# Kernel optimization log

Hardware: AMD Instinct MI355X
Metric: run time of the kernel (lower is better)

The kernel has to match this reference:

```python
import jax, jax.numpy as jnp
import numpy as np

B, N, C = 4, 1024, 1024
H = 16
HD = C // H
FF = 4 * C
EPS = 1e-6


def layernorm(x, g, b):
    mu = jnp.mean(x, axis=-1, keepdims=True)
    var = jnp.mean((x - mu) ** 2, axis=-1, keepdims=True)
    return (x - mu) * jax.lax.rsqrt(var + EPS) * g + b


def setup_inputs() -> dict:
    key = jax.random.key(0)
    ks = jax.random.split(key, 16)
    s = lambda fan_in: 1.0 / np.sqrt(fan_in)
    inp = {
        "x": jax.random.normal(ks[0], (B, N, C), dtype=jnp.float32),
        "qkv_w": jax.random.normal(ks[1], (3 * C, C), dtype=jnp.float32) * s(C),
        "qkv_b": jnp.zeros((3 * C,), jnp.float32),
        "attn_proj_w": jax.random.normal(ks[2], (C, C), dtype=jnp.float32) * s(C),
        "attn_proj_b": jnp.zeros((C,), jnp.float32),
        "blk_proj_w": jax.random.normal(ks[3], (C, C), dtype=jnp.float32) * s(C),
        "blk_proj_b": jnp.zeros((C,), jnp.float32),
        "ln1_g": jnp.ones((C,), jnp.float32),
        "ln1_b": jnp.zeros((C,), jnp.float32),
        "ln2_g": jnp.ones((C,), jnp.float32),
        "ln2_b": jnp.zeros((C,), jnp.float32),
        "fc1_w": jax.random.normal(ks[4], (FF, C), dtype=jnp.float32) * s(C),
        "fc1_b": jnp.zeros((FF,), jnp.float32),
        "fc2_w": jax.random.normal(ks[5], (C, FF), dtype=jnp.float32) * s(FF),
        "fc2_b": jnp.zeros((C,), jnp.float32),
        "mask": jnp.ones((B, N), jnp.int32),  # unused by the original forward
    }
    return inp


def reference(x, qkv_w, qkv_b, attn_proj_w, attn_proj_b, blk_proj_w, blk_proj_b,
              ln1_g, ln1_b, ln2_g, ln2_b, fc1_w, fc1_b, fc2_w, fc2_b, mask):
    shortcut = x
    xn = layernorm(x, ln1_g, ln1_b)

    # QKV projection: [B,N,3C] -> [3,B,H,N,HD]
    qkv = xn @ qkv_w.T + qkv_b
    qkv = qkv.reshape(B, N, 3, H, HD).transpose(2, 0, 3, 1, 4)
    q, k, v = qkv[0], qkv[1], qkv[2]
    scale = HD ** -0.5
    attn = jnp.einsum('bhqd,bhkd->bhqk', q * scale, k)
    attn = jax.nn.softmax(attn, axis=-1)
    o = jnp.einsum('bhqk,bhkd->bhqd', attn, v)
    o = o.transpose(0, 2, 1, 3).reshape(B, N, C)
    o = o @ attn_proj_w.T + attn_proj_b  # attention-internal proj

    x = shortcut + (o @ blk_proj_w.T + blk_proj_b)  # Block's extra proj + residual

    h = layernorm(x, ln2_g, ln2_b)
    h = jax.nn.gelu(h @ fc1_w.T + fc1_b, approximate=False)
    h = h @ fc2_w.T + fc2_b
    return x + h
```

## Files before the change

kernel.cpp:

```cpp
#include <hip/hip_runtime.h>

typedef unsigned short u16;
typedef __attribute__((ext_vector_type(8))) short short8;
typedef __attribute__((ext_vector_type(4))) float f32x4;

#define DEVI __device__ __forceinline__

static constexpr int Nn = 1024;
static constexpr int Cc = 1024;

DEVI u16 f2bf(float f) {
  union { float f; unsigned u; } v; v.f = f;
  unsigned r = v.u + 0x7fffu + ((v.u >> 16) & 1u);
  return (u16)(r >> 16);
}

DEVI void async_ld16(const void* g, void* lds) {
  __builtin_amdgcn_global_load_lds(
      (__attribute__((address_space(1))) void*)g,
      (__attribute__((address_space(3))) void*)lds, 16, 0, 0);
}

__global__ __launch_bounds__(256) void cvt_all(
    const float* __restrict__ s0, const float* __restrict__ s1,
    const float* __restrict__ s2, const float* __restrict__ s3,
    const float* __restrict__ s4, u16* __restrict__ out) {
  const size_t i = ((size_t)blockIdx.x * 256 + threadIdx.x) * 4;
  const float* src; size_t lo;
  if (i < 3145728)      { src = s0; lo = 0; }
  else if (i < 4194304) { src = s1; lo = 3145728; }
  else if (i < 5242880) { src = s2; lo = 4194304; }
  else if (i < 9437184) { src = s3; lo = 5242880; }
  else                  { src = s4; lo = 9437184; }
  const float4 v = *(const float4*)&src[i - lo];
  ushort4 o;
  o.x = f2bf(v.x); o.y = f2bf(v.y); o.z = f2bf(v.z); o.w = f2bf(v.w);
  *(ushort4*)&out[i] = o;
}

__global__ __launch_bounds__(256) void transpose_wT(const float* __restrict__ in,
                                                    u16* __restrict__ out) {
  __shared__ u16 tile[64][72];
  const int bx = blockIdx.x & 15, by = blockIdx.x >> 4;
  const int tr = threadIdx.x >> 2;
  const int tc4 = (threadIdx.x & 3) * 16;
#pragma unroll
  for (int j = 0; j < 4; ++j) {
    const float4 v = *(const float4*)&in[(size_t)(by * 64 + tr) * 1024 +
                                         bx * 64 + tc4 + j * 4];
    tile[tc4 + j * 4 + 0][tr] = f2bf(v.x);
    tile[tc4 + j * 4 + 1][tr] = f2bf(v.y);
    tile[tc4 + j * 4 + 2][tr] = f2bf(v.z);
    tile[tc4 + j * 4 + 3][tr] = f2bf(v.w);
  }
  __syncthreads();
#pragma unroll
  for (int j = 0; j < 4; ++j) {
    ushort4 o;
    o.x = tile[tr][tc4 + j * 4 + 0];
    o.y = tile[tr][tc4 + j * 4 + 1];
    o.z = tile[tr][tc4 + j * 4 + 2];
    o.w = tile[tr][tc4 + j * 4 + 3];
    *(ushort4*)&out[(size_t)(bx * 64 + tr) * 1024 + by * 64 + tc4 + j * 4] = o;
  }
}

__global__ __launch_bounds__(256) void cbias_k(const float* __restrict__ apb,
                                               const float* __restrict__ bpw,
                                               const float* __restrict__ bpb,
                                               float* __restrict__ cb) {
  const int j = blockIdx.x * 4 + (threadIdx.x >> 6);
  const int lane = threadIdx.x & 63;
  float s = 0.f;
  for (int k = lane; k < 1024; k += 64) s += apb[k] * bpw[(size_t)j * 1024 + k];
#pragma unroll
  for (int m = 1; m < 64; m <<= 1) s += __shfl_xor(s, m);
  if (lane == 0) cb[j] = s + bpb[j];
}

__global__ __launch_bounds__(256) void gemm64(const u16* __restrict__ A,
                                              const u16* __restrict__ W,
                                              u16* __restrict__ out, int K) {
  __shared__ __align__(16) u16 As[64 * 64];
  __shared__ __align__(16) u16 Bs[64 * 64];
  const int tid = threadIdx.x;
  const int wave = tid >> 6, lane = tid & 63;
  const int g = lane >> 4, lr = lane & 15;
  const int brow = (blockIdx.x >> 4) << 6, bcol = (blockIdx.x & 15) << 6;
  const int srow = lane >> 3;
  const int scg = (lane & 7) ^ srow;
  const int swz = (lr & 7) << 4;

  f32x4 acc[4];
#pragma unroll
  for (int j = 0; j < 4; ++j) acc[j] = (f32x4){0.f, 0.f, 0.f, 0.f};

  for (int k0 = 0; k0 < K; k0 += 64) {
#pragma unroll
    for (int u = 0; u < 2; ++u) {
      async_ld16(A + (size_t)(brow + u * 32 + wave * 8 + srow) * K + k0 + scg * 8,
                 (char*)As + u * 4096 + wave * 1024);
      async_ld16(W + (size_t)(bcol + u * 32 + wave * 8 + srow) * K + k0 + scg * 8,
                 (char*)Bs + u * 4096 + wave * 1024);
    }
    __syncthreads();
    short8 af[2], bf[4][2];
#pragma unroll
    for (int kk = 0; kk < 2; ++kk)
      af[kk] = *(const short8*)((char*)As + (wave * 16 + lr) * 128 +
                                ((kk * 64 + g * 16) ^ swz));
#pragma unroll
    for (int nf = 0; nf < 4; ++nf)
#pragma unroll
      for (int kk = 0; kk < 2; ++kk)
        bf[nf][kk] = *(const short8*)((char*)Bs + (nf * 16 + lr) * 128 +
                                      ((kk * 64 + g * 16) ^ swz));
#pragma unroll
    for (int nf = 0; nf < 4; ++nf)
#pragma unroll
      for (int kk = 0; kk < 2; ++kk)
        acc[nf] = __builtin_amdgcn_mfma_f32_16x16x32_bf16(af[kk], bf[nf][kk],
                                                          acc[nf], 0, 0, 0);
    __syncthreads();
  }
#pragma unroll
  for (int nf = 0; nf < 4; ++nf)
#pragma unroll
    for (int reg = 0; reg < 4; ++reg)
      out[(size_t)(brow + wave * 16 + g * 4 + reg) * 1024 +
          bcol + nf * 16 + lr] = f2bf(acc[nf][reg]);
}

__global__ __launch_bounds__(256) void vtrans(const u16* __restrict__ qkv,
                                              u16* __restrict__ vt) {
  __shared__ u16 tile[64][72];
  const int bh = blockIdx.x >> 4, tb = blockIdx.x & 15;
  const int b = bh >> 4, h = bh & 15;
  const int t0 = tb * 64;
  const int tid = threadIdx.x;
  const int rr = tid >> 3, c8 = (tid & 7) * 8;
#pragma unroll
  for (int r = 0; r < 2; ++r) {
    const int t = r * 32 + rr;
    const short8 v = *(const short8*)(qkv + (size_t)(b * Nn + t0 + t) * 3072 +
                                      2048 + h * 64 + c8);
#pragma unroll
    for (int j = 0; j < 8; ++j) tile[t][c8 + j] = (u16)v[j];
  }
  __syncthreads();
#pragma unroll
  for (int r = 0; r < 2; ++r) {
    const int d = r * 32 + rr;
    short8 o;
#pragma unroll
    for (int j = 0; j < 8; ++j) o[j] = (short)tile[c8 + j][d];
    *(short8*)(vt + (size_t)(bh * 64 + d) * 1024 + t0 + c8) = o;
  }
}

__global__ __launch_bounds__(256) void ln_bf16(const float* __restrict__ x,
                                               const float* __restrict__ gg,
                                               const float* __restrict__ bb,
                                               u16* __restrict__ out) {
  const int row = blockIdx.x;
  const float4 v = ((const float4*)(x + (size_t)row * 1024))[threadIdx.x];
  float s  = v.x + v.y + v.z + v.w;
  float s2 = v.x * v.x + v.y * v.y + v.z * v.z + v.w * v.w;
#pragma unroll
  for (int m = 1; m < 64; m <<= 1) { s += __shfl_xor(s, m); s2 += __shfl_xor(s2, m); }
  __shared__ float ps[4], ps2[4];
  const int wave = threadIdx.x >> 6;
  if ((threadIdx.x & 63) == 0) { ps[wave] = s; ps2[wave] = s2; }
  __syncthreads();
  s = ps[0] + ps[1] + ps[2] + ps[3];
  s2 = ps2[0] + ps2[1] + ps2[2] + ps2[3];
  const float mu = s * (1.0f / 1024.0f);
  const float var = s2 * (1.0f / 1024.0f) - mu * mu;
  const float rs = rsqrtf(var + 1e-6f);
  const float4 gv = ((const float4*)gg)[threadIdx.x];
  const float4 bv = ((const float4*)bb)[threadIdx.x];
  ushort4 o;
  o.x = f2bf((v.x - mu) * rs * gv.x + bv.x);
  o.y = f2bf((v.y - mu) * rs * gv.y + bv.y);
  o.z = f2bf((v.z - mu) * rs * gv.z + bv.z);
  o.w = f2bf((v.w - mu) * rs * gv.w + bv.w);
  ((ushort4*)(out + (size_t)row * 1024))[threadIdx.x] = o;
}

template <bool GELU_, bool OUTBF>
__global__ __launch_bounds__(512, 4) void gemmS(
    const u16* __restrict__ A, const u16* __restrict__ W,
    const float* __restrict__ bias, void* __restrict__ out,
    int M, int N, int K) {
  __shared__ __align__(16) u16 As[256 * 64];
  __shared__ __align__(16) u16 Bs[128 * 64];
  const int tid = threadIdx.x;
  const int wave = tid >> 6, lane = tid & 63;
  const int g = lane >> 4, lr = lane & 15;
  const int wm = wave >> 1, wn = wave & 1;
  const int ntile = N >> 7;
  const int nwg = gridDim.x;
  int bid = blockIdx.x;
  bid = (bid & 7) * (nwg >> 3) + (bid >> 3);
  const int brow = (bid / ntile) << 8, bcol = (bid % ntile) << 7;

  const int sru = wave * 8 + (lane >> 3);
  const int scg = (lane & 7) ^ (lane >> 3);
  const int swz = (lr & 7) << 4;

  f32x4 acc[4][4];
#pragma unroll
  for (int i = 0; i < 4; ++i)
#pragma unroll
    for (int j = 0; j < 4; ++j) acc[i][j] = (f32x4){0.f, 0.f, 0.f, 0.f};

  for (int k0 = 0; k0 < K; k0 += 64) {
#pragma unroll
    for (int u = 0; u < 2; ++u)
      async_ld16(W + (size_t)(bcol + u * 64 + sru) * K + k0 + scg * 8,
                 (char*)Bs + u * 8192 + wave * 1024);
#pragma unroll
    for (int u = 0; u < 4; ++u)
      async_ld16(A + (size_t)(brow + u * 64 + sru) * K + k0 + scg * 8,
                 (char*)As + u * 8192 + wave * 1024);
    asm volatile("s_waitcnt vmcnt(0)" ::: "memory");
    __builtin_amdgcn_s_barrier();

    short8 bf[4][2];
#pragma unroll
    for (int nf = 0; nf < 4; ++nf) {
      const int row = wn * 64 + nf * 16 + lr;
#pragma unroll
      for (int kk = 0; kk < 2; ++kk)
        bf[nf][kk] = *(const short8*)((const char*)Bs + row * 128 +
                                      ((kk * 64 + g * 16) ^ swz));
    }
    __builtin_amdgcn_s_setprio(1);
#pragma unroll
    for (int mf = 0; mf < 4; ++mf) {
      short8 af[2];
      const int row = wm * 64 + mf * 16 + lr;
#pragma unroll
      for (int kk = 0; kk < 2; ++kk)
        af[kk] = *(const short8*)((const char*)As + row * 128 +
                                  ((kk * 64 + g * 16) ^ swz));
#pragma unroll
      for (int nf = 0; nf < 4; ++nf)
#pragma unroll
        for (int kk = 0; kk < 2; ++kk)
          acc[mf][nf] = __builtin_amdgcn_mfma_f32_16x16x32_bf16(
              af[kk], bf[nf][kk], acc[mf][nf], 0, 0, 0);
    }
    __builtin_amdgcn_s_setprio(0);
    __builtin_amdgcn_s_barrier();
  }

#pragma unroll
  for (int mf = 0; mf < 4; ++mf)
#pragma unroll
    for (int nf = 0; nf < 4; ++nf) {
      const int cI = bcol + wn * 64 + nf * 16 + lr;
      const float bv = bias[cI];
#pragma unroll
      for (int reg = 0; reg < 4; ++reg) {
        const int r = brow + wm * 64 + mf * 16 + g * 4 + reg;
        float v = acc[mf][nf][reg] + bv;
        if (GELU_) v = 0.5f * v * (1.0f + erff(v * 0.70710678118654752f));
        if (OUTBF) ((u16*)out)[(size_t)r * N + cI] = f2bf(v);
        else       ((float*)out)[(size_t)r * N + cI] = v;
      }
    }
}

template <bool RESID, bool OUTBF>
__global__ __launch_bounds__(512, 2) void gemm128s(
    const u16* __restrict__ A, const u16* __restrict__ W,
    const float* __restrict__ bias, const float* __restrict__ resid,
    void* __restrict__ out, int M, int N, int K) {
  __shared__ __align__(16) u16 smem[32768];
  char* SA = (char*)smem;
  char* SB = SA + 32768;
  const int tid = threadIdx.x;
  const int wave = tid >> 6, lane = tid & 63;
  const int g = lane >> 4, lr = lane & 15;
  const int kg = wave & 1, ws = wave >> 1;
  const int wm = ws >> 1, wn = ws & 1;
  const int ntile = N >> 7;
  const int nwg = gridDim.x;
  int bid = blockIdx.x;
  bid = (bid & 7) * (nwg >> 3) + (bid >> 3);
  const int brow = (bid / ntile) << 7, bcol = (bid % ntile) << 7;

  const int sru = wave * 8 + (lane >> 3);
  const int scg = (lane & 7) ^ (lane >> 3);
  const int NT = K >> 6;

  f32x4 acc[4][4];
#pragma unroll
  for (int i = 0; i < 4; ++i)
#pragma unroll
    for (int j = 0; j < 4; ++j) acc[i][j] = (f32x4){0.f, 0.f, 0.f, 0.f};

  auto STA = [&](int s, int kt, int u) {
    async_ld16(A + (size_t)(brow + u * 64 + sru) * K + (size_t)kt * 64 + scg * 8,
               SA + s * 16384 + u * 8192 + wave * 1024);
  };
  auto STB = [&](int s, int kt, int u) {
    async_ld16(W + (size_t)(bcol + u * 64 + sru) * K + (size_t)kt * 64 + scg * 8,
               SB + s * 16384 + u * 8192 + wave * 1024);
  };

  const int colb = (kg * 64 + g * 16);
  const int swz = (lr & 7) << 4;

  STB(0, 0, 0); STB(0, 0, 1); STA(0, 0, 0); STA(0, 0, 1);
  asm volatile("s_waitcnt vmcnt(0)" ::: "memory");
  __builtin_amdgcn_s_barrier();

  for (int t = 0; t < NT; ++t) {
    const int c = t & 1, nc = c ^ 1;
    const int tn = (t + 1 < NT) ? t + 1 : t;
    const char* Ab = SA + c * 16384;
    const char* Bb = SB + c * 16384;

    short8 bf[4], af[2];
#pragma unroll
    for (int nf = 0; nf < 4; ++nf)
      bf[nf] = *(const short8*)(Bb + (wn * 64 + nf * 16 + lr) * 128 +
                                (colb ^ swz));
#pragma unroll
    for (int mf = 0; mf < 2; ++mf)
      af[mf] = *(const short8*)(Ab + (wm * 32 + mf * 16 + lr) * 128 +
                                (colb ^ swz));
    STB(nc, tn, 0); STB(nc, tn, 1);
    __builtin_amdgcn_s_setprio(1);
#pragma unroll
    for (int mf = 0; mf < 2; ++mf)
#pragma unroll
      for (int nf = 0; nf < 4; ++nf)
        acc[mf][nf] = __builtin_amdgcn_mfma_f32_16x16x32_bf16(
            af[mf], bf[nf], acc[mf][nf], 0, 0, 0);
    __builtin_amdgcn_s_setprio(0);
    asm volatile("s_waitcnt vmcnt(2)" ::: "memory");
    __builtin_amdgcn_s_barrier();

#pragma unroll
    for (int mf = 0; mf < 2; ++mf)
      af[mf] = *(const short8*)(Ab + (64 + wm * 32 + mf * 16 + lr) * 128 +
                                (colb ^ swz));
    STA(nc, tn, 0); STA(nc, tn, 1);
    __builtin_amdgcn_s_setprio(1);
#pragma unroll
    for (int mf = 0; mf < 2; ++mf)
#pragma unroll
      for (int nf = 0; nf < 4; ++nf)
        acc[mf + 2][nf] = __builtin_amdgcn_mfma_f32_16x16x32_bf16(
            af[mf], bf[nf], acc[mf + 2][nf], 0, 0, 0);
    __builtin_amdgcn_s_setprio(0);
    asm volatile("s_waitcnt vmcnt(1)" ::: "memory");
    __builtin_amdgcn_s_barrier();
  }

  asm volatile("s_waitcnt vmcnt(0)" ::: "memory");
  __syncthreads();
  float* pr = (float*)smem + (size_t)((wm << 1) | wn) * 4096;
  if (kg == 1) {
#pragma unroll
    for (int mf = 0; mf < 4; ++mf)
#pragma unroll
      for (int nf = 0; nf < 4; ++nf)
#pragma unroll
        for (int reg = 0; reg < 4; ++reg) {
          const int lrow = mf * 16 + g * 4 + reg;
          const int w = lrow * 64 +
                        ((nf * 16 + lr) ^ (g << 2) ^ ((g & 1) << 4));
          pr[w] = acc[mf][nf][reg];
        }
  }
  __syncthreads();
  if (kg == 0) {
#pragma unroll
    for (int mf = 0; mf < 4; ++mf) {
      const int rb = brow + ((mf < 2) ? wm * 32 + mf * 16
                                      : 64 + wm * 32 + (mf - 2) * 16);
#pragma unroll
      for (int nf = 0; nf < 4; ++nf) {
        const int cI = bcol + wn * 64 + nf * 16 + lr;
        const float bv = bias[cI];
#pragma unroll
        for (int reg = 0; reg < 4; ++reg) {
          const int lrow = mf * 16 + g * 4 + reg;
          const int w = lrow * 64 +
                        ((nf * 16 + lr) ^ (g << 2) ^ ((g & 1) << 4));
          const int r = rb + g * 4 + reg;
          float v = acc[mf][nf][reg] + pr[w] + bv;
          if (RESID) v += resid[(size_t)r * N + cI];
          if (OUTBF) ((u16*)out)[(size_t)r * N + cI] = f2bf(v);
          else       ((float*)out)[(size_t)r * N + cI] = v;
        }
      }
    }
  }
}

__global__ __launch_bounds__(256) void attn_kernel(const u16* __restrict__ qkv,
                                                   const u16* __restrict__ vt,
                                                   u16* __restrict__ o_out) {
  const int D = blockIdx.x;
  const int bh = (D & 7) + 8 * (D >> 7);
  const int qb = (D >> 3) & 15;
  const int b = bh >> 4, h = bh & 15;
  const int tid = threadIdx.x, wave = tid >> 6, lane = tid & 63;
  const int g = lane >> 4, lr = lane & 15;
  const u16* qg = qkv + (size_t)b * Nn * 3072 + h * 64;
  const u16* kg = qg + 1024;
  const u16* vgt = vt + (size_t)bh * 64 * 1024;

  __shared__ __align__(16) u16 Kl[64 * 64];
  __shared__ __align__(16) u16 Vt[64 * 64];
  __shared__ __align__(16) u16 Pl[64 * 64];

  const int q0 = qb * 64 + wave * 16;
  short8 qf[2];
#pragma unroll
  for (int kf = 0; kf < 2; ++kf)
    qf[kf] = *(const short8*)(qg + (size_t)(q0 + lr) * 3072 + kf * 32 + g * 8);

  f32x4 o[4];
  float ll[4];
#pragma unroll
  for (int df = 0; df < 4; ++df) o[df] = (f32x4){0.f, 0.f, 0.f, 0.f};
#pragma unroll
  for (int r = 0; r < 4; ++r) ll[r] = 0.f;

  for (int t0 = 0; t0 < Nn; t0 += 64) {
#pragma unroll
    for (int r = 0; r < 2; ++r) {
      const int c = r * 256 + wave * 64 + lane;
      const int t = c >> 3;
      const int ob = ((c & 7) << 4) ^ ((t & 7) << 4);
      async_ld16(kg + (size_t)(t0 + t) * 3072 + (ob >> 1),
                 (char*)Kl + (size_t)(r * 256 + wave * 64) * 16);
      async_ld16(vgt + (size_t)t * 1024 + t0 + (ob >> 1),
                 (char*)Vt + (size_t)(r * 256 + wave * 64) * 16);
    }
    __syncthreads();

    short8 kfr[4][2];
#pragma unroll
    for (int tf = 0; tf < 4; ++tf) {
      const int t = tf * 16 + lr;
#pragma unroll
      for (int kf = 0; kf < 2; ++kf)
        kfr[tf][kf] = *(const short8*)((const char*)Kl + t * 128 +
                                       ((kf * 64 + g * 16) ^ ((t & 7) << 4)));
    }
    f32x4 s[4];
    __builtin_amdgcn_s_setprio(1);
#pragma unroll
    for (int tf = 0; tf < 4; ++tf) {
      f32x4 z = (f32x4){0.f, 0.f, 0.f, 0.f};
      z = __builtin_amdgcn_mfma_f32_16x16x32_bf16(qf[0], kfr[tf][0], z, 0, 0, 0);
      z = __builtin_amdgcn_mfma_f32_16x16x32_bf16(qf[1], kfr[tf][1], z, 0, 0, 0);
      s[tf] = z;
    }
    __builtin_amdgcn_s_setprio(0);

    short8 vfr[4][2];
#pragma unroll
    for (int df = 0; df < 4; ++df) {
      const int d = df * 16 + lr;
#pragma unroll
      for (int kf = 0; kf < 2; ++kf)
        vfr[df][kf] = *(const short8*)((const char*)Vt + d * 128 +
                                       ((kf * 64 + g * 16) ^ ((d & 7) << 4)));
    }

#pragma unroll
    for (int tf = 0; tf < 4; ++tf)
#pragma unroll
      for (int reg = 0; reg < 4; ++reg) {
        const float p = __expf(s[tf][reg] * 0.125f);
        s[tf][reg] = p;
        ll[reg] += p;
      }

#pragma unroll
    for (int tf = 0; tf < 4; ++tf)
#pragma unroll
      for (int reg = 0; reg < 4; ++reg) {
        const int m = wave * 16 + g * 4 + reg;
        const int t2 = (tf * 16 + lr) * 2;
        *(u16*)((char*)Pl + m * 128 + (t2 ^ ((m & 7) << 4))) = f2bf(s[tf][reg]);
      }
    short8 pa[2];
#pragma unroll
    for (int kf = 0; kf < 2; ++kf)
      pa[kf] = *(const short8*)((const char*)Pl + (wave * 16 + lr) * 128 +
                                ((kf * 64 + g * 16) ^ ((lr & 7) << 4)));
    __builtin_amdgcn_s_setprio(1);
#pragma unroll
    for (int df = 0; df < 4; ++df) {
      o[df] = __builtin_amdgcn_mfma_f32_16x16x32_bf16(pa[0], vfr[df][0], o[df], 0, 0, 0);
      o[df] = __builtin_amdgcn_mfma_f32_16x16x32_bf16(pa[1], vfr[df][1], o[df], 0, 0, 0);
    }
    __builtin_amdgcn_s_setprio(0);
    __syncthreads();
  }

#pragma unroll
  for (int reg = 0; reg < 4; ++reg) {
#pragma unroll
    for (int msk = 1; msk < 16; msk <<= 1) ll[reg] += __shfl_xor(ll[reg], msk);
    const float inv = 1.0f / ll[reg];
    const int row = b * Nn + qb * 64 + wave * 16 + g * 4 + reg;
#pragma unroll
    for (int df = 0; df < 4; ++df) {
      const int col = h * 64 + df * 16 + lr;
      o_out[(size_t)row * 1024 + col] = f2bf(o[df][reg] * inv);
    }
  }
}

extern "C" void kernel_launch(void* const* d_in, const int* in_sizes, int n_in,
                              void* d_out, int out_size, void* d_ws, size_t ws_size,
                              hipStream_t stream) {
  const float* x    = (const float*)d_in[0];
  const float* qkvw = (const float*)d_in[1];
  const float* qkvb = (const float*)d_in[2];
  const float* apw  = (const float*)d_in[3];
  const float* apb  = (const float*)d_in[4];
  const float* bpw  = (const float*)d_in[5];
  const float* bpb  = (const float*)d_in[6];
  const float* ln1g = (const float*)d_in[7];
  const float* ln1b = (const float*)d_in[8];
  const float* ln2g = (const float*)d_in[9];
  const float* ln2b = (const float*)d_in[10];
  const float* fc1w = (const float*)d_in[11];
  const float* fc1b = (const float*)d_in[12];
  const float* fc2w = (const float*)d_in[13];
  const float* fc2b = (const float*)d_in[14];
  float* out = (float*)d_out;

  char* ws = (char*)d_ws;
  size_t off = 0;
  auto alloc = [&](size_t bytes) {
    char* p = ws + off;
    off += (bytes + 255) & ~(size_t)255;
    return p;
  };
  u16* wqkv  = (u16*)alloc((size_t)3145728 * 2);
  u16* wap   = (u16*)alloc((size_t)1048576 * 2);
  u16* wbp   = (u16*)alloc((size_t)1048576 * 2);
  u16* wfc1  = (u16*)alloc((size_t)4194304 * 2);
  u16* wfc2  = (u16*)alloc((size_t)4194304 * 2);
  u16* xn    = (u16*)alloc((size_t)4194304 * 2);
  u16* qkvbf = (u16*)alloc((size_t)12582912 * 2);
  u16* obuf  = (u16*)alloc((size_t)4194304 * 2);
  float* x2  = (float*)alloc((size_t)4194304 * 4);
  u16* wapT  = (u16*)alloc((size_t)1048576 * 2);
  u16* wc    = (u16*)alloc((size_t)1048576 * 2);
  float* cb  = (float*)alloc(1024 * 4);
  u16* vt    = (u16*)alloc((size_t)4194304 * 2);
  u16* ff    = qkvbf;
  (void)wap;

  cvt_all<<<13312, 256, 0, stream>>>(qkvw, apw, bpw, fc1w, fc2w, wqkv);
  transpose_wT<<<256, 256, 0, stream>>>(apw, wapT);
  cbias_k<<<256, 256, 0, stream>>>(apb, bpw, bpb, cb);

  gemm64<<<256, 256, 0, stream>>>(wbp, wapT, wc, 1024);

  ln_bf16<<<4096, 256, 0, stream>>>(x, ln1g, ln1b, xn);

  gemmS<false, true><<<384, 512, 0, stream>>>(
      xn, wqkv, qkvb, qkvbf, 4096, 3072, 1024);

  vtrans<<<1024, 256, 0, stream>>>(qkvbf, vt);

  attn_kernel<<<1024, 256, 0, stream>>>(qkvbf, vt, obuf);

  gemm128s<true, false><<<256, 512, 0, stream>>>(
      obuf, wc, cb, x, x2, 4096, 1024, 1024);

  ln_bf16<<<4096, 256, 0, stream>>>(x2, ln2g, ln2b, xn);

  gemmS<true, true><<<512, 512, 0, stream>>>(
      xn, wfc1, fc1b, ff, 4096, 4096, 1024);

  gemm128s<true, false><<<256, 512, 0, stream>>>(
      ff, wfc2, fc2b, x2, out, 4096, 1024, 4096);
}
```

Measured before the change: 236.5 us.

## Triple-buffer split-K 128x128 GEMM and skip converting unused attention-proj weights

The 128-tile GEMM used for the attention-output and fc2 projections moves from double buffering with two half-step barriers per K-tile to a three-stage ring. Each iteration prefetches the tile two steps ahead, does all 16 MFMAs, then waits and hits a single barrier. This is meant to hide global-load latency and halve barrier count, at the cost of 96KB LDS per block, which may reduce occupancy from two blocks per CU. The weight conversion kernel also skips the attention-proj weight, which is only used in transposed form, and the small gemm64 reorders its MFMA loop to interleave independent accumulators.

```diff
diff --git a/kernel.cpp b/kernel.cpp
--- a/kernel.cpp
+++ b/kernel.cpp
@@ -22,16 +22,18 @@
 }
 
 __global__ __launch_bounds__(256) void cvt_all(
-    const float* __restrict__ s0, const float* __restrict__ s1,
-    const float* __restrict__ s2, const float* __restrict__ s3,
-    const float* __restrict__ s4, u16* __restrict__ out) {
-  const size_t i = ((size_t)blockIdx.x * 256 + threadIdx.x) * 4;
-  const float* src; size_t lo;
-  if (i < 3145728)      { src = s0; lo = 0; }
-  else if (i < 4194304) { src = s1; lo = 3145728; }
-  else if (i < 5242880) { src = s2; lo = 4194304; }
-  else if (i < 9437184) { src = s3; lo = 5242880; }
-  else                  { src = s4; lo = 9437184; }
+    const float* __restrict__ s0, const float* __restrict__ s2,
+    const float* __restrict__ s3, const float* __restrict__ s4,
+    u16* __restrict__ out) {
+  const size_t j = ((size_t)blockIdx.x * 256 + threadIdx.x) * 4;
+  size_t i; const float* src; size_t lo;
+  if (j < 3145728) { i = j; src = s0; lo = 0; }
+  else {
+    i = j + 1048576;
+    if (i < 5242880)      { src = s2; lo = 4194304; }
+    else if (i < 9437184) { src = s3; lo = 5242880; }
+    else                  { src = s4; lo = 9437184; }
+  }
   const float4 v = *(const float4*)&src[i - lo];
   ushort4 o;
   o.x = f2bf(v.x); o.y = f2bf(v.y); o.z = f2bf(v.z); o.w = f2bf(v.w);
@@ -116,9 +118,9 @@
         bf[nf][kk] = *(const short8*)((char*)Bs + (nf * 16 + lr) * 128 +
                                       ((kk * 64 + g * 16) ^ swz));
 #pragma unroll
-    for (int nf = 0; nf < 4; ++nf)
-#pragma unroll
-      for (int kk = 0; kk < 2; ++kk)
+    for (int kk = 0; kk < 2; ++kk)
+#pragma unroll
+      for (int nf = 0; nf < 4; ++nf)
         acc[nf] = __builtin_amdgcn_mfma_f32_16x16x32_bf16(af[kk], bf[nf][kk],
                                                           acc[nf], 0, 0, 0);
     __syncthreads();
@@ -273,13 +275,11 @@
 }
 
 template <bool RESID, bool OUTBF>
-__global__ __launch_bounds__(512, 2) void gemm128s(
+__global__ __launch_bounds__(512, 2) void gemm128t(
     const u16* __restrict__ A, const u16* __restrict__ W,
     const float* __restrict__ bias, const float* __restrict__ resid,
     void* __restrict__ out, int M, int N, int K) {
-  __shared__ __align__(16) u16 smem[32768];
-  char* SA = (char*)smem;
-  char* SB = SA + 32768;
+  __shared__ __align__(16) u16 smem[49152];
   const int tid = threadIdx.x;
   const int wave = tid >> 6, lane = tid & 63;
   const int g = lane >> 4, lr = lane & 15;
@@ -301,63 +301,56 @@
 #pragma unroll
     for (int j = 0; j < 4; ++j) acc[i][j] = (f32x4){0.f, 0.f, 0.f, 0.f};
 
-  auto STA = [&](int s, int kt, int u) {
-    async_ld16(A + (size_t)(brow + u * 64 + sru) * K + (size_t)kt * 64 + scg * 8,
-               SA + s * 16384 + u * 8192 + wave * 1024);
+  auto STAGE = [&](int b, int kt) {
+    char* base = (char*)smem + b * 32768;
+#pragma unroll
+    for (int u = 0; u < 2; ++u)
+      async_ld16(W + (size_t)(bcol + u * 64 + sru) * K + (size_t)kt * 64 + scg * 8,
+                 base + 16384 + u * 8192 + wave * 1024);
+#pragma unroll
+    for (int u = 0; u < 2; ++u)
+      async_ld16(A + (size_t)(brow + u * 64 + sru) * K + (size_t)kt * 64 + scg * 8,
+                 base + u * 8192 + wave * 1024);
   };
-  auto STB = [&](int s, int kt, int u) {
-    async_ld16(W + (size_t)(bcol + u * 64 + sru) * K + (size_t)kt * 64 + scg * 8,
-               SB + s * 16384 + u * 8192 + wave * 1024);
-  };
-
-  const int colb = (kg * 64 + g * 16);
+
+  const int colb = kg * 64 + g * 16;
   const int swz = (lr & 7) << 4;
 
-  STB(0, 0, 0); STB(0, 0, 1); STA(0, 0, 0); STA(0, 0, 1);
-  asm volatile("s_waitcnt vmcnt(0)" ::: "memory");
+  STAGE(0, 0);
+  STAGE(1, 1 < NT ? 1 : 0);
+  asm volatile("s_waitcnt vmcnt(4)" ::: "memory");
   __builtin_amdgcn_s_barrier();
 
   for (int t = 0; t < NT; ++t) {
-    const int c = t & 1, nc = c ^ 1;
-    const int tn = (t + 1 < NT) ? t + 1 : t;
-    const char* Ab = SA + c * 16384;
-    const char* Bb = SB + c * 16384;
-
-    short8 bf[4], af[2];
+    const int b = t % 3;
+    const char* Ab = (const char*)smem + b * 32768;
+    const char* Bb = Ab + 16384;
+
+    short8 bf[4], af[4];
 #pragma unroll
     for (int nf = 0; nf < 4; ++nf)
       bf[nf] = *(const short8*)(Bb + (wn * 64 + nf * 16 + lr) * 128 +
                                 (colb ^ swz));
 #pragma unroll
-    for (int mf = 0; mf < 2; ++mf)
-      af[mf] = *(const short8*)(Ab + (wm * 32 + mf * 16 + lr) * 128 +
-                                (colb ^ swz));
-    STB(nc, tn, 0); STB(nc, tn, 1);
+    for (int mf = 0; mf < 2; ++mf) {
+      af[mf]     = *(const short8*)(Ab + (wm * 32 + mf * 16 + lr) * 128 +
+                                    (colb ^ swz));
+      af[mf + 2] = *(const short8*)(Ab + (64 + wm * 32 + mf * 16 + lr) * 128 +
+                                    (colb ^ swz));
+    }
+    {
+      const int pt = (t + 2 < NT) ? t + 2 : NT - 1;
+      STAGE((t + 2) % 3, pt);
+    }
     __builtin_amdgcn_s_setprio(1);
 #pragma unroll
-    for (int mf = 0; mf < 2; ++mf)
+    for (int mf = 0; mf < 4; ++mf)
 #pragma unroll
       for (int nf = 0; nf < 4; ++nf)
         acc[mf][nf] = __builtin_amdgcn_mfma_f32_16x16x32_bf16(
             af[mf], bf[nf], acc[mf][nf], 0, 0, 0);
     __builtin_amdgcn_s_setprio(0);
-    asm volatile("s_waitcnt vmcnt(2)" ::: "memory");
-    __builtin_amdgcn_s_barrier();
-
-#pragma unroll
-    for (int mf = 0; mf < 2; ++mf)
-      af[mf] = *(const short8*)(Ab + (64 + wm * 32 + mf * 16 + lr) * 128 +
-                                (colb ^ swz));
-    STA(nc, tn, 0); STA(nc, tn, 1);
-    __builtin_amdgcn_s_setprio(1);
-#pragma unroll
-    for (int mf = 0; mf < 2; ++mf)
-#pragma unroll
-      for (int nf = 0; nf < 4; ++nf)
-        acc[mf + 2][nf] = __builtin_amdgcn_mfma_f32_16x16x32_bf16(
-            af[mf], bf[nf], acc[mf + 2][nf], 0, 0, 0);
-    __builtin_amdgcn_s_setprio(0);
-    asm volatile("s_waitcnt vmcnt(1)" ::: "memory");
+    asm volatile("s_waitcnt vmcnt(4)" ::: "memory");
     __builtin_amdgcn_s_barrier();
   }
 
@@ -565,7 +558,7 @@
   u16* ff    = qkvbf;
   (void)wap;
 
-  cvt_all<<<13312, 256, 0, stream>>>(qkvw, apw, bpw, fc1w, fc2w, wqkv);
+  cvt_all<<<12288, 256, 0, stream>>>(qkvw, bpw, fc1w, fc2w, wqkv);
   transpose_wT<<<256, 256, 0, stream>>>(apw, wapT);
   cbias_k<<<256, 256, 0, stream>>>(apb, bpw, bpb, cb);
 
@@ -580,7 +573,7 @@
 
   attn_kernel<<<1024, 256, 0, stream>>>(qkvbf, vt, obuf);
 
-  gemm128s<true, false><<<256, 512, 0, stream>>>(
+  gemm128t<true, false><<<256, 512, 0, stream>>>(
       obuf, wc, cb, x, x2, 4096, 1024, 1024);
 
   ln_bf16<<<4096, 256, 0, stream>>>(x2, ln2g, ln2b, xn);
@@ -588,6 +581,6 @@
   gemmS<true, true><<<512, 512, 0, stream>>>(
       xn, wfc1, fc1b, ff, 4096, 4096, 1024);
 
-  gemm128s<true, false><<<256, 512, 0, stream>>>(
+  gemm128t<true, false><<<256, 512, 0, stream>>>(
       ff, wfc2, fc2b, x2, out, 4096, 1024, 4096);
 }
```

Result: faster. 226.5 us (-4.3%).
